# Optimization experiments

Hardware: AMD Instinct MI355X
Metric: run time of the kernel (lower is better)

## Reference

```python
import jax, jax.numpy as jnp
import numpy as np

N_NODES = 50000
N_EDGES = 800000
D_IN = 96
HID = 128


def _glorot(key, shape):
    fan_in, fan_out = shape[0], shape[1]
    lim = np.sqrt(6.0 / (fan_in + fan_out)).astype(np.float32)
    return jax.random.uniform(key, shape, jnp.float32, -lim, lim)


def setup_inputs() -> dict:
    key = jax.random.key(0)
    ks = jax.random.split(key, 12)
    x = jax.random.normal(ks[0], (N_NODES, D_IN), jnp.float32)
    edge_index = jax.random.randint(ks[1], (2, N_EDGES), 0, N_NODES)
    return {
        "x": x,
        "edge_index": edge_index,
        "W_in": _glorot(ks[2], (D_IN, HID)),
        "b_in": jnp.zeros((HID,), jnp.float32),
        "W1": _glorot(ks[3], (HID, HID)),
        "b1": jnp.zeros((HID,), jnp.float32),
        "W2": _glorot(ks[4], (HID, HID)),
        "b2": jnp.zeros((HID,), jnp.float32),
        "Wm1": _glorot(ks[5], (2 * HID, HID)),
        "bm1": jnp.zeros((HID,), jnp.float32),
        "Wm2": _glorot(ks[6], (HID, 1)),
        "bm2": jnp.zeros((1,), jnp.float32),
    }


def _gcn_conv(h, W, b, src, dst, n_nodes):
    # PyG GCNConv with add_self_loops=True, normalize=True:
    # out = D^{-1/2} (A + I) D^{-1/2} (h W) + b, aggregating x_j (source) into dst.
    loop = jnp.arange(n_nodes)
    row = jnp.concatenate([src, loop])  # source / j
    col = jnp.concatenate([dst, loop])  # target / i
    deg = jax.ops.segment_sum(jnp.ones(row.shape, h.dtype), col, num_segments=n_nodes)
    dinv = jnp.where(deg > 0, jax.lax.rsqrt(deg), 0.0)
    norm = dinv[row] * dinv[col]  # [E+N]
    xw = h @ W  # [N, H]
    msg = xw[row] * norm[:, None]  # gather + scale, [E+N, H]
    out = jax.ops.segment_sum(msg, col, num_segments=n_nodes)  # scatter-add
    return out + b


def reference(x, edge_index, W_in, b_in, W1, b1, W2, b2, Wm1, bm1, Wm2, bm2):
    src, dst = edge_index[0], edge_index[1]
    n = x.shape[0]
    h = jax.nn.relu(x @ W_in + b_in)  # dropout is identity at inference
    h = jax.nn.relu(_gcn_conv(h, W1, b1, src, dst, n))
    h = jax.nn.relu(_gcn_conv(h, W2, b2, src, dst, n))
    ef = jnp.concatenate([h[src], h[dst]], axis=1)  # [E, 2H]
    hid = jax.nn.relu(ef @ Wm1 + bm1)
    logits = (hid @ Wm2 + bm2)[:, 0]  # [E]
    return logits
```

## Files before the change

### kernel.cpp

```cpp
#include <hip/hip_runtime.h>

#define N_NODES 50000
#define N_EDGES 800000
#define D_IN 96
#define HID 128
#define NB 391
#define BCAP 3072

typedef __attribute__((ext_vector_type(8))) _Float16 halfx8;
typedef __attribute__((ext_vector_type(4))) _Float16 half4v;
typedef __attribute__((ext_vector_type(2))) _Float16 half2v;
typedef __attribute__((ext_vector_type(16))) float f32x16;

__global__ __launch_bounds__(256) void bucket_hist_kernel(const int* __restrict__ dst,
                                                          int* __restrict__ bhist) {
    __shared__ int lh[NB];
    int t = threadIdx.x;
    for (int i = t; i < NB; i += 256) lh[i] = 0;
    __syncthreads();
    int base = blockIdx.x * 4096;
#pragma unroll
    for (int i = 0; i < 16; i++) {
        int e = base + i * 256 + t;
        if (e < N_EDGES) atomicAdd(&lh[dst[e] >> 7], 1);
    }
    __syncthreads();
    for (int i = t; i < NB; i += 256) atomicAdd(&bhist[i], lh[i]);
}

__global__ __launch_bounds__(512) void scan_buckets_kernel(const int* __restrict__ bhist,
                                                           int* __restrict__ boff,
                                                           int* __restrict__ bcursor) {
    __shared__ int s[512];
    int t = threadIdx.x;
    int v = (t < NB) ? bhist[t] : 0;
    s[t] = v;
    __syncthreads();
    for (int off = 1; off < 512; off <<= 1) {
        int u = (t >= off) ? s[t - off] : 0;
        __syncthreads();
        s[t] += u;
        __syncthreads();
    }
    if (t < NB) {
        int ex = s[t] - v;
        boff[t] = ex;
        bcursor[t] = ex;
    }
    if (t == NB - 1) boff[NB] = s[t];
}

__global__ __launch_bounds__(512) void bin_kernel(const int* __restrict__ src,
                                                  const int* __restrict__ dst,
                                                  int* __restrict__ bcursor,
                                                  unsigned long long* __restrict__ binned) {
    __shared__ int lh[NB];
    __shared__ int gbs[NB];
    int t = threadIdx.x;
    for (int i = t; i < NB; i += 512) lh[i] = 0;
    __syncthreads();
    int base = blockIdx.x * 8192;
    unsigned long long pk[16];
    int bb[16], rk[16];
#pragma unroll
    for (int i = 0; i < 16; i++) {
        int e = base + i * 512 + t;
        bb[i] = -1;
        if (e < N_EDGES) {
            int s = src[e], d = dst[e];
            int b = d >> 7;
            bb[i] = b;
            pk[i] = ((unsigned long long)s << 27) |
                    ((unsigned long long)(d & 127) << 20) | (unsigned long long)e;
            rk[i] = atomicAdd(&lh[b], 1);
        }
    }
    __syncthreads();
    for (int i = t; i < NB; i += 512) gbs[i] = atomicAdd(&bcursor[i], lh[i]);
    __syncthreads();
#pragma unroll
    for (int i = 0; i < 16; i++) {
        if (bb[i] >= 0) binned[gbs[bb[i]] + rk[i]] = pk[i];
    }
}

__global__ __launch_bounds__(256) void bucket_sort_kernel(const unsigned long long* __restrict__ binned,
                                                          const int* __restrict__ boff,
                                                          int* __restrict__ ce_src,
                                                          int* __restrict__ ce_eid,
                                                          int* __restrict__ ce_dst,
                                                          int* __restrict__ csr_ptr,
                                                          float* __restrict__ dinv) {
    __shared__ unsigned long long ed[BCAP];
    __shared__ int2 sorted[BCAP];
    __shared__ int cntA[128], sc[128];
    int b = blockIdx.x;
    int t = threadIdx.x;
    int base = boff[b];
    int k = boff[b + 1] - base;
    if (k > BCAP) k = BCAP;
    if (t < 128) cntA[t] = 0;
    __syncthreads();
    int rk[12], li[12];
    int nmine = 0;
    for (int i = t; i < k; i += 256) {
        unsigned long long p = binned[base + i];
        ed[i] = p;
        int d = (int)((p >> 20) & 127);
        rk[nmine] = atomicAdd(&cntA[d], 1);
        li[nmine] = i;
        nmine++;
    }
    __syncthreads();
    if (t < 128) sc[t] = cntA[t];
    __syncthreads();
    for (int off = 1; off < 128; off <<= 1) {
        int u = 0;
        if (t < 128 && t >= off) u = sc[t - off];
        __syncthreads();
        if (t < 128) sc[t] += u;
        __syncthreads();
    }
    for (int m = 0; m < nmine; m++) {
        unsigned long long p = ed[li[m]];
        int d = (int)((p >> 20) & 127);
        int pos = sc[d] - cntA[d] + rk[m];
        int srcn = (int)(p >> 27);
        int eid = (int)(p & 0xFFFFF);
        sorted[pos] = make_int2(srcn | (d << 16), eid);
    }
    __syncthreads();
    for (int i = t; i < k; i += 256) {
        int2 se = sorted[i];
        ce_src[base + i] = se.x & 0xFFFF;
        ce_eid[base + i] = se.y;
        ce_dst[base + i] = (b << 7) + (se.x >> 16);
    }
    if (t < 128) {
        int node = (b << 7) + t;
        if (node < N_NODES) {
            csr_ptr[node] = base + sc[t] - cntA[t];
            dinv[node] = 1.0f / sqrtf((float)(cntA[t] + 1));
        }
    }
    if (b == NB - 1 && t == 0) csr_ptr[N_NODES] = boff[NB];
}

__global__ __launch_bounds__(256) void pack_weights_kernel(const float* __restrict__ W_in,
                                                           const float* __restrict__ W1,
                                                           const float* __restrict__ W2,
                                                           const float* __restrict__ Wm1,
                                                           _Float16* __restrict__ packed) {
    int t = blockIdx.x * 256 + threadIdx.x;
    const float* Wsrc;
    int K, u;
    if (t < 12288)      { Wsrc = W_in;            K = 96;  u = t; }
    else if (t < 28672) { Wsrc = W1;              K = 128; u = t - 12288; }
    else if (t < 45056) { Wsrc = W2;              K = 128; u = t - 28672; }
    else if (t < 61440) { Wsrc = Wm1;             K = 128; u = t - 45056; }
    else                { Wsrc = Wm1 + 128 * 128; K = 128; u = t - 61440; }
    if (t >= 77824) return;
    int steps = K >> 4;
    int cb = u / (steps * 512);
    int rem = u - cb * steps * 512;
    int s = rem >> 9;
    int lane = (rem >> 3) & 63;
    int j = rem & 7;
    int k = s * 16 + ((lane >> 5) << 3) + j;
    int n = (cb << 5) + (lane & 31);
    packed[t] = (_Float16)Wsrc[k * 128 + n];
}

__global__ __launch_bounds__(256) void fused_in_kernel(const float* __restrict__ x,
                                                       const _Float16* __restrict__ WpIn,
                                                       const _Float16* __restrict__ Wp1,
                                                       const float* __restrict__ b_in,
                                                       const float* __restrict__ dinv,
                                                       _Float16* __restrict__ y1, int M) {
    __shared__ _Float16 As[32 * 104];
    __shared__ _Float16 Hs[32 * 136];
    int tid = threadIdx.x;
    int M0 = blockIdx.x * 32;
    for (int i = tid; i < 32 * 24; i += 256) {
        int r = i / 24, c = i - r * 24;
        float4 v = make_float4(0.f, 0.f, 0.f, 0.f);
        int row = M0 + r;
        if (row < M) v = *(const float4*)&x[(size_t)row * 96 + c * 4];
        half2v a = {(_Float16)v.x, (_Float16)v.y};
        half2v b = {(_Float16)v.z, (_Float16)v.w};
        *(half2v*)&As[r * 104 + c * 4] = a;
        *(half2v*)&As[r * 104 + c * 4 + 2] = b;
    }
    __syncthreads();

    int wave = tid >> 6, lane = tid & 63;
    int col = wave * 32 + (lane & 31);
    {
        const halfx8* bp = (const halfx8*)WpIn + (size_t)wave * 6 * 64 + lane;
        const _Float16* arow = &As[(lane & 31) * 104 + ((lane >> 5) << 3)];
        f32x16 acc = {};
#pragma unroll
        for (int s = 0; s < 6; s++) {
            halfx8 a = *(const halfx8*)&arow[s * 16];
            acc = __builtin_amdgcn_mfma_f32_32x32x16_f16(a, bp[s * 64], acc, 0, 0, 0);
        }
        float bA = b_in[col];
#pragma unroll
        for (int r = 0; r < 16; r++) {
            int rl = (r & 3) + 8 * (r >> 2) + 4 * (lane >> 5);
            Hs[rl * 136 + col] = (_Float16)fmaxf(acc[r] + bA, 0.f);
        }
    }
    __syncthreads();
    {
        const halfx8* bp = (const halfx8*)Wp1 + (size_t)wave * 8 * 64 + lane;
        const _Float16* arow = &Hs[(lane & 31) * 136 + ((lane >> 5) << 3)];
        f32x16 acc = {};
#pragma unroll
        for (int s = 0; s < 8; s++) {
            halfx8 a = *(const halfx8*)&arow[s * 16];
            acc = __builtin_amdgcn_mfma_f32_32x32x16_f16(a, bp[s * 64], acc, 0, 0, 0);
        }
#pragma unroll
        for (int r = 0; r < 16; r++) {
            int rl = (r & 3) + 8 * (r >> 2) + 4 * (lane >> 5);
            int grow = M0 + rl;
            if (grow < M) {
                y1[(size_t)grow * 128 + col] = (_Float16)(acc[r] * dinv[grow]);
            }
        }
    }
}

__global__ __launch_bounds__(256) void gemm_f16_kernel(const _Float16* __restrict__ A,
                                                       const _Float16* __restrict__ Wp,
                                                       const float* __restrict__ bias,
                                                       const float* __restrict__ rowscale,
                                                       _Float16* __restrict__ out,
                                                       int M, int K, int steps, int dorelu) {
    __shared__ _Float16 As[32 * 136];
    int tid = threadIdx.x;
    int M0 = blockIdx.x * 32;
    int stride = K + 8;
    int CH = K >> 3;
    int tot = 32 * CH;
    for (int i = tid; i < tot; i += 256) {
        int r = i / CH, c = i - r * CH;
        uint4 v = make_uint4(0, 0, 0, 0);
        int row = M0 + r;
        if (row < M) v = *(const uint4*)&A[(size_t)row * K + c * 8];
        *(uint4*)&As[r * stride + c * 8] = v;
    }
    __syncthreads();

    int wave = tid >> 6, lane = tid & 63;
    const halfx8* bp = (const halfx8*)Wp + (size_t)wave * steps * 64 + lane;
    const _Float16* arow = &As[(lane & 31) * stride + ((lane >> 5) << 3)];
    f32x16 acc = {};
    for (int s = 0; s < steps; s++) {
        halfx8 a = *(const halfx8*)&arow[s * 16];
        acc = __builtin_amdgcn_mfma_f32_32x32x16_f16(a, bp[s * 64], acc, 0, 0, 0);
    }
    int col = wave * 32 + (lane & 31);
    float bA = bias ? bias[col] : 0.f;
#pragma unroll
    for (int r = 0; r < 16; r++) {
        int rl = (r & 3) + 8 * (r >> 2) + 4 * (lane >> 5);
        int grow = M0 + rl;
        if (grow < M) {
            float sc = rowscale ? rowscale[grow] : 1.f;
            float v0 = (acc[r] + bA) * sc;
            if (dorelu) v0 = fmaxf(v0, 0.f);
            out[(size_t)grow * 128 + col] = (_Float16)v0;
        }
    }
}

__global__ __launch_bounds__(256) void gemm_uv_kernel(const _Float16* __restrict__ A,
                                                      const _Float16* __restrict__ WpU,
                                                      const _Float16* __restrict__ WpV,
                                                      const float* __restrict__ bm1,
                                                      _Float16* __restrict__ U,
                                                      _Float16* __restrict__ V,
                                                      int M) {
    const int K = 128, steps = 8;
    __shared__ _Float16 As[32 * 136];
    int tid = threadIdx.x;
    int M0 = blockIdx.x * 32;
    int stride = K + 8;
    for (int i = tid; i < 32 * 16; i += 256) {
        int r = i >> 4, c = i & 15;
        uint4 v = make_uint4(0, 0, 0, 0);
        int row = M0 + r;
        if (row < M) v = *(const uint4*)&A[(size_t)row * K + c * 8];
        *(uint4*)&As[r * stride + c * 8] = v;
    }
    __syncthreads();

    int wave = tid >> 6, lane = tid & 63;
    const halfx8* bu = (const halfx8*)WpU + (size_t)wave * steps * 64 + lane;
    const halfx8* bv = (const halfx8*)WpV + (size_t)wave * steps * 64 + lane;
    const _Float16* arow = &As[(lane & 31) * stride + ((lane >> 5) << 3)];
    f32x16 au = {}, av = {};
#pragma unroll
    for (int s = 0; s < steps; s++) {
        halfx8 a = *(const halfx8*)&arow[s * 16];
        au = __builtin_amdgcn_mfma_f32_32x32x16_f16(a, bu[s * 64], au, 0, 0, 0);
        av = __builtin_amdgcn_mfma_f32_32x32x16_f16(a, bv[s * 64], av, 0, 0, 0);
    }
    int col = wave * 32 + (lane & 31);
    float bA = bm1[col];
#pragma unroll
    for (int r = 0; r < 16; r++) {
        int rl = (r & 3) + 8 * (r >> 2) + 4 * (lane >> 5);
        int grow = M0 + rl;
        if (grow < M) {
            U[(size_t)grow * 128 + col] = (_Float16)(au[r] + bA);
            V[(size_t)grow * 128 + col] = (_Float16)av[r];
        }
    }
}

__global__ __launch_bounds__(256) void aggregate_kernel(const _Float16* __restrict__ y,
                                                        const float* __restrict__ dinv,
                                                        const int* __restrict__ ptr,
                                                        const int* __restrict__ ce_src,
                                                        const float* __restrict__ bias,
                                                        _Float16* __restrict__ out) {
    int node = blockIdx.x * 8 + (threadIdx.x >> 5);
    int l = threadIdx.x & 31;
    float di = dinv[node];
    half4v self = ((const half4v*)&y[(size_t)node * 128])[l];
    float a0 = (float)self[0], a1 = (float)self[1], a2 = (float)self[2], a3 = (float)self[3];
    float b0 = 0.f, b1 = 0.f, b2 = 0.f, b3 = 0.f;
    int s0 = ptr[node], s1 = ptr[node + 1];
    int j = s0;
    for (; j + 7 < s1; j += 8) {
        int n0 = ce_src[j], n1 = ce_src[j + 1], n2 = ce_src[j + 2], n3 = ce_src[j + 3];
        int n4 = ce_src[j + 4], n5 = ce_src[j + 5], n6 = ce_src[j + 6], n7 = ce_src[j + 7];
        half4v v0 = ((const half4v*)&y[(size_t)n0 * 128])[l];
        half4v v1 = ((const half4v*)&y[(size_t)n1 * 128])[l];
        half4v v2 = ((const half4v*)&y[(size_t)n2 * 128])[l];
        half4v v3 = ((const half4v*)&y[(size_t)n3 * 128])[l];
        half4v v4 = ((const half4v*)&y[(size_t)n4 * 128])[l];
        half4v v5 = ((const half4v*)&y[(size_t)n5 * 128])[l];
        half4v v6 = ((const half4v*)&y[(size_t)n6 * 128])[l];
        half4v v7 = ((const half4v*)&y[(size_t)n7 * 128])[l];
        a0 += (float)v0[0] + (float)v2[0] + (float)v4[0] + (float)v6[0];
        a1 += (float)v0[1] + (float)v2[1] + (float)v4[1] + (float)v6[1];
        a2 += (float)v0[2] + (float)v2[2] + (float)v4[2] + (float)v6[2];
        a3 += (float)v0[3] + (float)v2[3] + (float)v4[3] + (float)v6[3];
        b0 += (float)v1[0] + (float)v3[0] + (float)v5[0] + (float)v7[0];
        b1 += (float)v1[1] + (float)v3[1] + (float)v5[1] + (float)v7[1];
        b2 += (float)v1[2] + (float)v3[2] + (float)v5[2] + (float)v7[2];
        b3 += (float)v1[3] + (float)v3[3] + (float)v5[3] + (float)v7[3];
    }
    for (; j < s1; j++) {
        int n = ce_src[j];
        half4v v = ((const half4v*)&y[(size_t)n * 128])[l];
        a0 += (float)v[0]; a1 += (float)v[1]; a2 += (float)v[2]; a3 += (float)v[3];
    }
    float4 bv = *(const float4*)&bias[l * 4];
    half4v ov;
    ov[0] = (_Float16)fmaxf(di * (a0 + b0) + bv.x, 0.f);
    ov[1] = (_Float16)fmaxf(di * (a1 + b1) + bv.y, 0.f);
    ov[2] = (_Float16)fmaxf(di * (a2 + b2) + bv.z, 0.f);
    ov[3] = (_Float16)fmaxf(di * (a3 + b3) + bv.w, 0.f);
    ((half4v*)&out[(size_t)node * 128])[l] = ov;
}

__global__ __launch_bounds__(256) void edge_mlp_kernel(const _Float16* __restrict__ Ub,
                                                       const _Float16* __restrict__ Vb,
                                                       const int* __restrict__ ce_src,
                                                       const int* __restrict__ ce_eid,
                                                       const int* __restrict__ ce_dst,
                                                       const float* __restrict__ Wm2,
                                                       const float* __restrict__ bm2,
                                                       float* __restrict__ out) {
    __shared__ int ssrc[64], sdst[64], seid[64];
    int tid = threadIdx.x;
    int e0 = blockIdx.x * 64;
    if (tid < 64) {
        ssrc[tid] = ce_src[e0 + tid];
        seid[tid] = ce_eid[e0 + tid];
    } else if (tid < 128) {
        sdst[tid - 64] = ce_dst[e0 + tid - 64];
    }
    __syncthreads();
    int g = tid >> 4;
    int l = tid & 15;
    int ga = g, gb = g + 16, gc = g + 32, gd = g + 48;
    halfx8 u0 = *(const halfx8*)&Ub[(size_t)ssrc[ga] * 128 + l * 8];
    halfx8 v0 = *(const halfx8*)&Vb[(size_t)sdst[ga] * 128 + l * 8];
    halfx8 u1 = *(const halfx8*)&Ub[(size_t)ssrc[gb] * 128 + l * 8];
    halfx8 v1 = *(const halfx8*)&Vb[(size_t)sdst[gb] * 128 + l * 8];
    halfx8 u2 = *(const halfx8*)&Ub[(size_t)ssrc[gc] * 128 + l * 8];
    halfx8 v2 = *(const halfx8*)&Vb[(size_t)sdst[gc] * 128 + l * 8];
    halfx8 u3 = *(const halfx8*)&Ub[(size_t)ssrc[gd] * 128 + l * 8];
    halfx8 v3 = *(const halfx8*)&Vb[(size_t)sdst[gd] * 128 + l * 8];
    float4 w0 = *(const float4*)&Wm2[l * 8];
    float4 w1 = *(const float4*)&Wm2[l * 8 + 4];
    float wm[8] = {w0.x, w0.y, w0.z, w0.w, w1.x, w1.y, w1.z, w1.w};
    float p0 = 0.f, p1 = 0.f, p2 = 0.f, p3 = 0.f;
#pragma unroll
    for (int t = 0; t < 8; t++) {
        p0 = fmaf(fmaxf((float)u0[t] + (float)v0[t], 0.f), wm[t], p0);
        p1 = fmaf(fmaxf((float)u1[t] + (float)v1[t], 0.f), wm[t], p1);
        p2 = fmaf(fmaxf((float)u2[t] + (float)v2[t], 0.f), wm[t], p2);
        p3 = fmaf(fmaxf((float)u3[t] + (float)v3[t], 0.f), wm[t], p3);
    }
#pragma unroll
    for (int d = 1; d < 16; d <<= 1) {
        p0 += __shfl_xor(p0, d);
        p1 += __shfl_xor(p1, d);
        p2 += __shfl_xor(p2, d);
        p3 += __shfl_xor(p3, d);
    }
    if (l == 0) {
        float bb = bm2[0];
        out[seid[ga]] = p0 + bb;
        out[seid[gb]] = p1 + bb;
        out[seid[gc]] = p2 + bb;
        out[seid[gd]] = p3 + bb;
    }
}

extern "C" void kernel_launch(void* const* d_in, const int* in_sizes, int n_in,
                              void* d_out, int out_size, void* d_ws, size_t ws_size,
                              hipStream_t stream) {
    const float* x    = (const float*)d_in[0];
    const int* eidx   = (const int*)d_in[1];
    const float* W_in = (const float*)d_in[2];
    const float* b_in = (const float*)d_in[3];
    const float* W1   = (const float*)d_in[4];
    const float* b1   = (const float*)d_in[5];
    const float* W2   = (const float*)d_in[6];
    const float* b2   = (const float*)d_in[7];
    const float* Wm1  = (const float*)d_in[8];
    const float* bm1  = (const float*)d_in[9];
    const float* Wm2  = (const float*)d_in[10];
    const float* bm2  = (const float*)d_in[11];
    float* out = (float*)d_out;
    const int* src = eidx;
    const int* dst = eidx + N_EDGES;

    char* w = (char*)d_ws;
    size_t off = 0;
    auto alloc = [&](size_t bytes) -> char* {
        char* p = w + off;
        off = (off + bytes + 255) & ~(size_t)255;
        return p;
    };
    int* bhist    = (int*)alloc((size_t)NB * 4);
    int* boff     = (int*)alloc((size_t)(NB + 1) * 4);
    int* bcursor  = (int*)alloc((size_t)NB * 4);
    int* csr_ptr  = (int*)alloc((size_t)(N_NODES + 1) * 4);
    float* dinv   = (float*)alloc((size_t)N_NODES * 4);
    unsigned long long* binned = (unsigned long long*)alloc((size_t)N_EDGES * 8);
    int* ce_src   = (int*)alloc((size_t)N_EDGES * 4);
    int* ce_eid   = (int*)alloc((size_t)N_EDGES * 4);
    int* ce_dst   = (int*)alloc((size_t)N_EDGES * 4);
    _Float16* Wp  = (_Float16*)alloc((size_t)77824 * 2);
    _Float16* y1  = (_Float16*)alloc((size_t)N_NODES * HID * 2);
    _Float16* y2  = (_Float16*)alloc((size_t)N_NODES * HID * 2);
    _Float16* hbuf = (_Float16*)alloc((size_t)N_NODES * HID * 2);
    _Float16* Ub  = (_Float16*)alloc((size_t)N_NODES * HID * 2);
    _Float16* Vb  = (_Float16*)alloc((size_t)N_NODES * HID * 2);

    const _Float16* WpIn  = Wp;
    const _Float16* Wp1   = Wp + 12288;
    const _Float16* Wp2   = Wp + 28672;
    const _Float16* WpM1a = Wp + 45056;
    const _Float16* WpM1b = Wp + 61440;

    hipMemsetAsync(bhist, 0, (size_t)NB * 4, stream);
    bucket_hist_kernel<<<196, 256, 0, stream>>>(dst, bhist);
    scan_buckets_kernel<<<1, 512, 0, stream>>>(bhist, boff, bcursor);
    bin_kernel<<<98, 512, 0, stream>>>(src, dst, bcursor, binned);
    bucket_sort_kernel<<<NB, 256, 0, stream>>>(binned, boff, ce_src, ce_eid, ce_dst,
                                               csr_ptr, dinv);
    pack_weights_kernel<<<(77824 + 255) / 256, 256, 0, stream>>>(W_in, W1, W2, Wm1, Wp);

    int gblocks = (N_NODES + 31) / 32;
    fused_in_kernel<<<gblocks, 256, 0, stream>>>(x, WpIn, Wp1, b_in, dinv, y1, N_NODES);
    aggregate_kernel<<<N_NODES / 8, 256, 0, stream>>>(y1, dinv, csr_ptr, ce_src, b1, hbuf);
    gemm_f16_kernel<<<gblocks, 256, 0, stream>>>(hbuf, Wp2, nullptr, dinv, y2,
                                                 N_NODES, HID, 8, 0);
    aggregate_kernel<<<N_NODES / 8, 256, 0, stream>>>(y2, dinv, csr_ptr, ce_src, b2, hbuf);
    gemm_uv_kernel<<<gblocks, 256, 0, stream>>>(hbuf, WpM1a, WpM1b, bm1, Ub, Vb, N_NODES);
    edge_mlp_kernel<<<N_EDGES / 64, 256, 0, stream>>>(Ub, Vb, ce_src, ce_eid, ce_dst,
                                                      Wm2, bm2, out);
}
```

Baseline: 260.3 us.

## Fuse histogram with weight packing; widen edge MLP to 128 edges with packed f16 dot2

```diff
diff --git a/kernel.cpp b/kernel.cpp
--- a/kernel.cpp
+++ b/kernel.cpp
@@ -12,20 +12,67 @@
 typedef __attribute__((ext_vector_type(2))) _Float16 half2v;
 typedef __attribute__((ext_vector_type(16))) float f32x16;
 
-__global__ __launch_bounds__(256) void bucket_hist_kernel(const int* __restrict__ dst,
-                                                          int* __restrict__ bhist) {
+__device__ inline float dot2acc(half2v a, half2v b, float c) {
+#if __has_builtin(__builtin_amdgcn_fdot2)
+    return __builtin_amdgcn_fdot2(a, b, c, false);
+#else
+    return c + (float)a[0] * (float)b[0] + (float)a[1] * (float)b[1];
+#endif
+}
+
+__device__ inline halfx8 relu8(halfx8 s) {
+#if __has_builtin(__builtin_elementwise_max)
+    return __builtin_elementwise_max(s, (halfx8)0);
+#else
+    halfx8 r;
+#pragma unroll
+    for (int i = 0; i < 8; i++) r[i] = s[i] > (_Float16)0 ? s[i] : (_Float16)0;
+    return r;
+#endif
+}
+
+__global__ __launch_bounds__(256) void hist_pack_kernel(const int* __restrict__ dst,
+                                                        int* __restrict__ bhist,
+                                                        const float* __restrict__ W_in,
+                                                        const float* __restrict__ W1,
+                                                        const float* __restrict__ W2,
+                                                        const float* __restrict__ Wm1,
+                                                        const float* __restrict__ Wm2,
+                                                        _Float16* __restrict__ packed) {
     __shared__ int lh[NB];
     int t = threadIdx.x;
-    for (int i = t; i < NB; i += 256) lh[i] = 0;
-    __syncthreads();
-    int base = blockIdx.x * 4096;
-#pragma unroll
-    for (int i = 0; i < 16; i++) {
-        int e = base + i * 256 + t;
-        if (e < N_EDGES) atomicAdd(&lh[dst[e] >> 7], 1);
-    }
-    __syncthreads();
-    for (int i = t; i < NB; i += 256) atomicAdd(&bhist[i], lh[i]);
+    if (blockIdx.x < 196) {
+        for (int i = t; i < NB; i += 256) lh[i] = 0;
+        __syncthreads();
+        int base = blockIdx.x * 4096;
+#pragma unroll
+        for (int i = 0; i < 16; i++) {
+            int e = base + i * 256 + t;
+            if (e < N_EDGES) atomicAdd(&lh[dst[e] >> 7], 1);
+        }
+        __syncthreads();
+        for (int i = t; i < NB; i += 256) atomicAdd(&bhist[i], lh[i]);
+        return;
+    }
+    int g = (blockIdx.x - 196) * 256 + t;
+    if (g >= 77952) return;
+    if (g >= 77824) { packed[g] = (_Float16)Wm2[g - 77824]; return; }
+    const float* Wsrc;
+    int K, u;
+    if (g < 12288)      { Wsrc = W_in;            K = 96;  u = g; }
+    else if (g < 28672) { Wsrc = W1;              K = 128; u = g - 12288; }
+    else if (g < 45056) { Wsrc = W2;              K = 128; u = g - 28672; }
+    else if (g < 61440) { Wsrc = Wm1;             K = 128; u = g - 45056; }
+    else                { Wsrc = Wm1 + 128 * 128; K = 128; u = g - 61440; }
+    int steps = K >> 4;
+    int cb = u / (steps * 512);
+    int rem = u - cb * steps * 512;
+    int s = rem >> 9;
+    int lane = (rem >> 3) & 63;
+    int j = rem & 7;
+    int k = s * 16 + ((lane >> 5) << 3) + j;
+    int n = (cb << 5) + (lane & 31);
+    packed[g] = (_Float16)Wsrc[k * 128 + n];
 }
 
 __global__ __launch_bounds__(512) void scan_buckets_kernel(const int* __restrict__ bhist,
@@ -144,31 +191,6 @@
         }
     }
     if (b == NB - 1 && t == 0) csr_ptr[N_NODES] = boff[NB];
-}
-
-__global__ __launch_bounds__(256) void pack_weights_kernel(const float* __restrict__ W_in,
-                                                           const float* __restrict__ W1,
-                                                           const float* __restrict__ W2,
-                                                           const float* __restrict__ Wm1,
-                                                           _Float16* __restrict__ packed) {
-    int t = blockIdx.x * 256 + threadIdx.x;
-    const float* Wsrc;
-    int K, u;
-    if (t < 12288)      { Wsrc = W_in;            K = 96;  u = t; }
-    else if (t < 28672) { Wsrc = W1;              K = 128; u = t - 12288; }
-    else if (t < 45056) { Wsrc = W2;              K = 128; u = t - 28672; }
-    else if (t < 61440) { Wsrc = Wm1;             K = 128; u = t - 45056; }
-    else                { Wsrc = Wm1 + 128 * 128; K = 128; u = t - 61440; }
-    if (t >= 77824) return;
-    int steps = K >> 4;
-    int cb = u / (steps * 512);
-    int rem = u - cb * steps * 512;
-    int s = rem >> 9;
-    int lane = (rem >> 3) & 63;
-    int j = rem & 7;
-    int k = s * 16 + ((lane >> 5) << 3) + j;
-    int n = (cb << 5) + (lane & 31);
-    packed[t] = (_Float16)Wsrc[k * 128 + n];
 }
 
 __global__ __launch_bounds__(256) void fused_in_kernel(const float* __restrict__ x,
@@ -374,54 +396,49 @@
                                                        const int* __restrict__ ce_src,
                                                        const int* __restrict__ ce_eid,
                                                        const int* __restrict__ ce_dst,
-                                                       const float* __restrict__ Wm2,
+                                                       const _Float16* __restrict__ Wm2h,
                                                        const float* __restrict__ bm2,
                                                        float* __restrict__ out) {
-    __shared__ int ssrc[64], sdst[64], seid[64];
+    __shared__ int ssrc[128], sdst[128], seid[128];
     int tid = threadIdx.x;
-    int e0 = blockIdx.x * 64;
-    if (tid < 64) {
+    int e0 = blockIdx.x * 128;
+    if (tid < 128) {
         ssrc[tid] = ce_src[e0 + tid];
         seid[tid] = ce_eid[e0 + tid];
-    } else if (tid < 128) {
-        sdst[tid - 64] = ce_dst[e0 + tid - 64];
+    } else {
+        sdst[tid - 128] = ce_dst[e0 + tid - 128];
     }
     __syncthreads();
     int g = tid >> 4;
     int l = tid & 15;
-    int ga = g, gb = g + 16, gc = g + 32, gd = g + 48;
-    halfx8 u0 = *(const halfx8*)&Ub[(size_t)ssrc[ga] * 128 + l * 8];
-    halfx8 v0 = *(const halfx8*)&Vb[(size_t)sdst[ga] * 128 + l * 8];
-    halfx8 u1 = *(const halfx8*)&Ub[(size_t)ssrc[gb] * 128 + l * 8];
-    halfx8 v1 = *(const halfx8*)&Vb[(size_t)sdst[gb] * 128 + l * 8];
-    halfx8 u2 = *(const halfx8*)&Ub[(size_t)ssrc[gc] * 128 + l * 8];
-    halfx8 v2 = *(const halfx8*)&Vb[(size_t)sdst[gc] * 128 + l * 8];
-    halfx8 u3 = *(const halfx8*)&Ub[(size_t)ssrc[gd] * 128 + l * 8];
-    halfx8 v3 = *(const halfx8*)&Vb[(size_t)sdst[gd] * 128 + l * 8];
-    float4 w0 = *(const float4*)&Wm2[l * 8];
-    float4 w1 = *(const float4*)&Wm2[l * 8 + 4];
-    float wm[8] = {w0.x, w0.y, w0.z, w0.w, w1.x, w1.y, w1.z, w1.w};
-    float p0 = 0.f, p1 = 0.f, p2 = 0.f, p3 = 0.f;
-#pragma unroll
-    for (int t = 0; t < 8; t++) {
-        p0 = fmaf(fmaxf((float)u0[t] + (float)v0[t], 0.f), wm[t], p0);
-        p1 = fmaf(fmaxf((float)u1[t] + (float)v1[t], 0.f), wm[t], p1);
-        p2 = fmaf(fmaxf((float)u2[t] + (float)v2[t], 0.f), wm[t], p2);
-        p3 = fmaf(fmaxf((float)u3[t] + (float)v3[t], 0.f), wm[t], p3);
+    halfx8 wv = *(const halfx8*)&Wm2h[l * 8];
+    half2v w0 = {wv[0], wv[1]}, w1 = {wv[2], wv[3]}, w2 = {wv[4], wv[5]}, w3 = {wv[6], wv[7]};
+    halfx8 uu[8], vv[8];
+#pragma unroll
+    for (int k = 0; k < 8; k++) {
+        int e = g + 16 * k;
+        uu[k] = *(const halfx8*)&Ub[(size_t)ssrc[e] * 128 + l * 8];
+        vv[k] = *(const halfx8*)&Vb[(size_t)sdst[e] * 128 + l * 8];
+    }
+    float p[8];
+#pragma unroll
+    for (int k = 0; k < 8; k++) {
+        halfx8 s = relu8(uu[k] + vv[k]);
+        half2v s0 = {s[0], s[1]}, s1 = {s[2], s[3]}, s2 = {s[4], s[5]}, s3 = {s[6], s[7]};
+        float acc = dot2acc(s0, w0, 0.f);
+        acc = dot2acc(s1, w1, acc);
+        acc = dot2acc(s2, w2, acc);
+        p[k] = dot2acc(s3, w3, acc);
     }
 #pragma unroll
     for (int d = 1; d < 16; d <<= 1) {
-        p0 += __shfl_xor(p0, d);
-        p1 += __shfl_xor(p1, d);
-        p2 += __shfl_xor(p2, d);
-        p3 += __shfl_xor(p3, d);
+#pragma unroll
+        for (int k = 0; k < 8; k++) p[k] += __shfl_xor(p[k], d);
     }
     if (l == 0) {
         float bb = bm2[0];
-        out[seid[ga]] = p0 + bb;
-        out[seid[gb]] = p1 + bb;
-        out[seid[gc]] = p2 + bb;
-        out[seid[gd]] = p3 + bb;
+#pragma unroll
+        for (int k = 0; k < 8; k++) out[seid[g + 16 * k]] = p[k] + bb;
     }
 }
 
@@ -460,7 +477,7 @@
     int* ce_src   = (int*)alloc((size_t)N_EDGES * 4);
     int* ce_eid   = (int*)alloc((size_t)N_EDGES * 4);
     int* ce_dst   = (int*)alloc((size_t)N_EDGES * 4);
-    _Float16* Wp  = (_Float16*)alloc((size_t)77824 * 2);
+    _Float16* Wp  = (_Float16*)alloc((size_t)77952 * 2);
     _Float16* y1  = (_Float16*)alloc((size_t)N_NODES * HID * 2);
     _Float16* y2  = (_Float16*)alloc((size_t)N_NODES * HID * 2);
     _Float16* hbuf = (_Float16*)alloc((size_t)N_NODES * HID * 2);
@@ -472,14 +489,14 @@
     const _Float16* Wp2   = Wp + 28672;
     const _Float16* WpM1a = Wp + 45056;
     const _Float16* WpM1b = Wp + 61440;
+    const _Float16* Wm2h  = Wp + 77824;
 
     hipMemsetAsync(bhist, 0, (size_t)NB * 4, stream);
-    bucket_hist_kernel<<<196, 256, 0, stream>>>(dst, bhist);
+    hist_pack_kernel<<<196 + 305, 256, 0, stream>>>(dst, bhist, W_in, W1, W2, Wm1, Wm2, Wp);
     scan_buckets_kernel<<<1, 512, 0, stream>>>(bhist, boff, bcursor);
     bin_kernel<<<98, 512, 0, stream>>>(src, dst, bcursor, binned);
     bucket_sort_kernel<<<NB, 256, 0, stream>>>(binned, boff, ce_src, ce_eid, ce_dst,
                                                csr_ptr, dinv);
-    pack_weights_kernel<<<(77824 + 255) / 256, 256, 0, stream>>>(W_in, W1, W2, Wm1, Wp);
 
     int gblocks = (N_NODES + 31) / 32;
     fused_in_kernel<<<gblocks, 256, 0, stream>>>(x, WpIn, Wp1, b_in, dinv, y1, N_NODES);
@@ -488,6 +505,6 @@
                                                  N_NODES, HID, 8, 0);
     aggregate_kernel<<<N_NODES / 8, 256, 0, stream>>>(y2, dinv, csr_ptr, ce_src, b2, hbuf);
     gemm_uv_kernel<<<gblocks, 256, 0, stream>>>(hbuf, WpM1a, WpM1b, bm1, Ub, Vb, N_NODES);
-    edge_mlp_kernel<<<N_EDGES / 64, 256, 0, stream>>>(Ub, Vb, ce_src, ce_eid, ce_dst,
-                                                      Wm2, bm2, out);
-}
+    edge_mlp_kernel<<<N_EDGES / 128, 256, 0, stream>>>(Ub, Vb, ce_src, ce_eid, ce_dst,
+                                                       Wm2h, bm2, out);
+}
```

Measured after the change: 256.5 us. No clear change (-1.5%).
